# Kernel tuning notes

Measured on AMD Instinct MI355X. Metric: run time of the kernel, lower is better.

Reference implementation:

```python
import jax, jax.numpy as jnp
import numpy as np

N_HEAD = 16
HEAD_DIM = 64


def _shift(BD):
    # BD: [b, n, L, 2L] -> [b, n, L, L] (Transformer-XL left-shift trick)
    b, n, L, _ = BD.shape
    BD = jnp.pad(BD, ((0, 0), (0, 0), (0, 0), (0, 1)))          # [b,n,L,2L+1]
    BD = BD.reshape(b, n, 2 * L + 1, L)[:, :, :-1]              # [b,n,2L,L]
    BD = BD.reshape(b, n, L, 2 * L)[:, :, :, L:]                # [b,n,L,L]
    return BD


def _transpose_shift(E):
    # E: [b, n, L, 2L] -> [b, n, L, L]
    b, n, L, _ = E.shape
    E = jnp.pad(E, ((0, 0), (0, 0), (0, 0), (0, 1)))            # [b,n,L,2L+1]
    E = E.reshape(b, n, 2 * L + 1, L)                           # [b,n,2L+1,L]
    E = E[:, :, 1::2, :]                                        # rows 1,3,...,2L-1 -> [b,n,L,L]
    return E


def setup_inputs() -> dict:
    key = jax.random.key(0)
    ks = jax.random.split(key, 6)
    B, L, D = 4, 1024, 1024
    return {
        "x": jax.random.normal(ks[0], (B, L, D), jnp.float32),
        "pos_embed": jax.random.normal(ks[1], (2 * L, HEAD_DIM), jnp.float32),
        "W_qkv": jax.random.normal(ks[2], (D, 3 * D), jnp.float32) * (1.0 / np.sqrt(D)),
        "b_qkv": jax.random.normal(ks[3], (3 * D,), jnp.float32) * 0.01,
        "r_r_bias": jax.random.normal(ks[4], (N_HEAD, HEAD_DIM), jnp.float32) * 0.02,
        "r_w_bias": jax.random.normal(ks[5], (N_HEAD, HEAD_DIM), jnp.float32) * 0.02,
    }


def reference(x, pos_embed, W_qkv, b_qkv, r_r_bias, r_w_bias):
    b, L, d_model = x.shape
    scale = jnp.sqrt(jnp.asarray(HEAD_DIM, x.dtype))

    qkv = x @ W_qkv + b_qkv                                      # [b,L,3D]
    q, k, v = jnp.split(qkv, 3, axis=-1)

    def split_heads(t):  # [b,L,D] -> [b,n,L,hd]
        return t.reshape(b, L, N_HEAD, HEAD_DIM).transpose(0, 2, 1, 3)

    q, k, v = split_heads(q), split_heads(k), split_heads(v)

    rw_head_q = q + r_r_bias[None, :, None, :]
    AC = jnp.einsum('bnqd,bnkd->bnqk', rw_head_q, k)             # [b,n,L,L]
    D_ = jnp.einsum('nd,ld->nl', r_w_bias, pos_embed)[None, :, None, :]  # [1,n,1,2L]
    B_ = jnp.einsum('bnqd,ld->bnql', q, pos_embed)               # [b,n,L,2L]
    E_ = jnp.einsum('bnqd,ld->bnql', k, pos_embed)               # [b,n,L,2L]

    BDE = _shift(B_ + D_) + _transpose_shift(E_)
    attn = jax.nn.softmax((AC + BDE) / scale, axis=-1)

    out = jnp.einsum('bnqk,bnkd->bnqd', attn, v)                 # [b,n,L,hd]
    out = out.transpose(0, 2, 1, 3).reshape(b, L, d_model)       # merge heads
    return out
```

## Files before the change

kernel.cpp:

```cpp
#include <hip/hip_runtime.h>
#include <math.h>

typedef unsigned short u16;
typedef unsigned int u32;
typedef __attribute__((ext_vector_type(8))) short bf16x8;
typedef __attribute__((ext_vector_type(4))) float f32x4;

#define AS1 __attribute__((address_space(1)))
#define AS3 __attribute__((address_space(3)))

static __device__ __forceinline__ u16 f2b(float f) {
  u32 u = __float_as_uint(f);
  return (u16)((u + 0x7FFFu + ((u >> 16) & 1u)) >> 16);
}
static __device__ __forceinline__ u16 f2b_fast(float f) {
  return (u16)((__float_as_uint(f) + 0x8000u) >> 16);
}
static __device__ __forceinline__ float b2f(u16 b) {
  return __uint_as_float(((u32)b) << 16);
}

__global__ __launch_bounds__(256) void prep(
    const float* __restrict__ x, const float* __restrict__ W,
    const float* __restrict__ P,
    u16* __restrict__ xb, u16* __restrict__ Wt, u16* __restrict__ Pb)
{
  __shared__ u16 sT[64 * 68];
  const int bid = blockIdx.x, t = threadIdx.x;
  if (bid < 4096) {
    const size_t base = (size_t)bid * 1024 + t * 4;
    const float4 v = *(const float4*)(x + base);
    const u32 lo = (u32)f2b(v.x) | ((u32)f2b(v.y) << 16);
    const u32 hi = (u32)f2b(v.z) | ((u32)f2b(v.w) << 16);
    *(uint2*)(xb + base) = make_uint2(lo, hi);
  } else if (bid < 4224) {
    const size_t base = (size_t)(bid - 4096) * 1024 + t * 4;
    const float4 v = *(const float4*)(P + base);
    const u32 lo = (u32)f2b(v.x) | ((u32)f2b(v.y) << 16);
    const u32 hi = (u32)f2b(v.z) | ((u32)f2b(v.w) << 16);
    *(uint2*)(Pb + base) = make_uint2(lo, hi);
  } else if (bid < 4992) {
    const int tb = bid - 4224;
    const int tk = tb / 48, tn = tb % 48;
    const int k0 = tk * 64, n0 = tn * 64;
#pragma unroll
    for (int it = 0; it < 4; ++it) {
      const int c = it * 256 + t;
      const int r = c >> 4, c4 = (c & 15) << 2;
      const float4 v = *(const float4*)(W + (size_t)(k0 + r) * 3072 + n0 + c4);
      sT[(c4 + 0) * 68 + r] = f2b(v.x);
      sT[(c4 + 1) * 68 + r] = f2b(v.y);
      sT[(c4 + 2) * 68 + r] = f2b(v.z);
      sT[(c4 + 3) * 68 + r] = f2b(v.w);
    }
    __syncthreads();
#pragma unroll
    for (int it = 0; it < 4; ++it) {
      const int c = it * 256 + t;
      const int rr = c >> 4, k4 = (c & 15) << 2;
      const uint2 rv = *(const uint2*)(sT + rr * 68 + k4);
      *(uint2*)(Wt + (size_t)(n0 + rr) * 1024 + k0 + k4) = rv;
    }
  } else {
    if (t < 64) Pb[2048 * 64 + t] = f2b(P[2047 * 64 + t]);
  }
}

__global__ __launch_bounds__(256, 3) void qkv_gemm(
    const u16* __restrict__ xb, const u16* __restrict__ Wt,
    const float* __restrict__ bq,
    u16* __restrict__ Qh, u16* __restrict__ Kh, u16* __restrict__ Vt)
{
  __shared__ u16 smem[16384];
  u16* const sA = smem;
  u16* const sB = smem + 8192;
  u16* const T  = smem;
  u16* const Tv = smem;
  const int t = threadIdx.x;
  const int lane = t & 63, w = t >> 6;
  const int l = lane & 15, ql = lane >> 4;
  const int wm = w & 1, wn = w >> 1;
  const int vid = blockIdx.x;
  const int xcd = vid & 7, jj = vid >> 3;
  const int n0 = (xcd * 3 + (jj % 3)) * 128;
  const int m0 = (jj / 3) * 128;

  f32x4 acc[4][4];
#pragma unroll
  for (int i = 0; i < 4; ++i)
#pragma unroll
    for (int j = 0; j < 4; ++j) acc[i][j] = (f32x4){0.f, 0.f, 0.f, 0.f};

  for (int k0 = 0; k0 < 1024; k0 += 64) {
    __syncthreads();
#pragma unroll
    for (int j = 0; j < 4; ++j) {
      const int ii = w * 4 + j;
      const int m = ii * 8 + (lane >> 3);
      const int q8 = (lane & 7) ^ (m & 7);
      __builtin_amdgcn_global_load_lds(
          (const AS1 u32*)(xb + (size_t)(m0 + m) * 1024 + k0 + q8 * 8),
          (AS3 u32*)(sA + ii * 512), 16, 0, 0);
      __builtin_amdgcn_global_load_lds(
          (const AS1 u32*)(Wt + (size_t)(n0 + m) * 1024 + k0 + q8 * 8),
          (AS3 u32*)(sB + ii * 512), 16, 0, 0);
    }
    __syncthreads();
#pragma unroll
    for (int ks = 0; ks < 2; ++ks) {
      bf16x8 a[4], b[4];
#pragma unroll
      for (int mt = 0; mt < 4; ++mt) {
        const int m = wm * 64 + mt * 16 + l;
        a[mt] = *(const bf16x8*)(sA + m * 64 + (((ks * 4 + ql) ^ (m & 7)) * 8));
      }
#pragma unroll
      for (int nt = 0; nt < 4; ++nt) {
        const int nn = wn * 64 + nt * 16 + l;
        b[nt] = *(const bf16x8*)(sB + nn * 64 + (((ks * 4 + ql) ^ (nn & 7)) * 8));
      }
#pragma unroll
      for (int mt = 0; mt < 4; ++mt)
#pragma unroll
        for (int nt = 0; nt < 4; ++nt)
          acc[mt][nt] = __builtin_amdgcn_mfma_f32_16x16x32_bf16(
              a[mt], b[nt], acc[mt][nt], 0, 0, 0);
    }
  }

  const int which = n0 >> 10;
  const int qbase = m0 & 1023;
  const int bb = m0 >> 10;
  const int h0 = (n0 & 1023) >> 6;
#pragma unroll
  for (int pass = 0; pass < 2; ++pass) {
    __syncthreads();
    if (which < 2) {
      if (wm == pass) {
#pragma unroll
        for (int nt = 0; nt < 4; ++nt) {
          const int col = wn * 64 + nt * 16 + l;
          const float bias = bq[n0 + col];
#pragma unroll
          for (int mt = 0; mt < 4; ++mt)
#pragma unroll
            for (int rg = 0; rg < 4; ++rg)
              T[(mt * 16 + ql * 4 + rg) * 136 + col] = f2b(acc[mt][nt][rg] + bias);
        }
      }
      __syncthreads();
      u16* const dst = which ? Kh : Qh;
#pragma unroll
      for (int h = 0; h < 2; ++h) {
        const size_t bnoff = ((size_t)(bb * 16 + h0 + h)) << 16;
#pragma unroll
        for (int it = 0; it < 2; ++it) {
          const int c = it * 256 + t;
          const int r = c >> 3, d8 = (c & 7) * 8;
          const uint4 v = *(const uint4*)(T + r * 136 + h * 64 + d8);
          *(uint4*)(dst + bnoff + ((size_t)(qbase + pass * 64 + r) << 6) + d8) = v;
        }
      }
    } else {
      if (wm == pass) {
#pragma unroll
        for (int nt = 0; nt < 4; ++nt) {
          const int col = wn * 64 + nt * 16 + l;
          const float bias = bq[n0 + col];
#pragma unroll
          for (int mt = 0; mt < 4; ++mt) {
            const u32 lo = (u32)f2b(acc[mt][nt][0] + bias) |
                           ((u32)f2b(acc[mt][nt][1] + bias) << 16);
            const u32 hi = (u32)f2b(acc[mt][nt][2] + bias) |
                           ((u32)f2b(acc[mt][nt][3] + bias) << 16);
            *(uint2*)(Tv + col * 72 + mt * 16 + ql * 4) = make_uint2(lo, hi);
          }
        }
      }
      __syncthreads();
#pragma unroll
      for (int h = 0; h < 2; ++h) {
        const size_t bnoff = ((size_t)(bb * 16 + h0 + h)) << 16;
#pragma unroll
        for (int it = 0; it < 2; ++it) {
          const int c = it * 256 + t;
          const int dr = c >> 3, q8 = (c & 7) * 8;
          const uint4 v = *(const uint4*)(Tv + (h * 64 + dr) * 72 + q8);
          *(uint4*)(Vt + bnoff + ((size_t)dr << 10) + qbase + pass * 64 + q8) = v;
        }
      }
    }
  }
}

__global__ __launch_bounds__(256, 2) void rel_attn(
    const u16* __restrict__ Qh, const u16* __restrict__ Kh,
    const u16* __restrict__ Vt, const u16* __restrict__ Pb,
    const float* __restrict__ rrb, const float* __restrict__ rwb,
    float* __restrict__ out)
{
  __shared__ u16 smem[36864];
  u16* const sK    = smem;
  u16* const sVT   = smem + 8192;
  u16* const sPr   = smem + 16384;
  u16* const sProb = smem + 32768;
  u16* const sU    = smem;
  u16* const sW    = smem + 16384;

  const int t = threadIdx.x;
  const int lane = t & 63, w = t >> 6;
  const int l = lane & 15, ql = lane >> 4;
  const int vid = blockIdx.x;
  const int qt = vid >> 6, bn = vid & 63;
  const int n = bn & 15, bb = bn >> 4;
  const size_t hoff = (size_t)bn << 16;
  const int q0 = qt << 7;
  const int bz = 6 - 2 * w;

#pragma unroll
  for (int it = 0; it < 4; ++it) {
    const int c = it * 256 + t;
    const int i = c >> 3, ch = c & 7;
    const int d8 = ch * 8;
    const uint4 qv = *(const uint4*)(Qh + hoff + ((size_t)(q0 + i) << 6) + d8);
    const uint4 kv = *(const uint4*)(Kh + hoff + ((size_t)(q0 + i) << 6) + d8);
    const u16* qp = (const u16*)&qv;
    const u16* kp = (const u16*)&kv;
    u16 uo[8], wo[8];
#pragma unroll
    for (int e = 0; e < 8; ++e) {
      const float rv = rrb[n * 64 + d8 + e];
      const float wv = rwb[n * 64 + d8 + e];
      const float qf = b2f(qp[e]), kf = b2f(kp[e]);
      uo[e] = f2b(qf + rv);
      wo[e] = f2b(qf + wv + kf);
    }
    const int pos = i * 64 + ((ch ^ (i & 7)) * 8);
    *(uint4*)(sU + pos) = *(const uint4*)uo;
    *(uint4*)(sW + pos) = *(const uint4*)wo;
  }
  __syncthreads();

  bf16x8 au[2][2], aw[2][2];
#pragma unroll
  for (int mt = 0; mt < 2; ++mt)
#pragma unroll
    for (int ks = 0; ks < 2; ++ks) {
      const int row = w * 32 + mt * 16 + l;
      const int off = row * 64 + (((ks * 4 + ql) ^ (row & 7)) * 8);
      au[mt][ks] = *(const bf16x8*)(sU + off);
      aw[mt][ks] = *(const bf16x8*)(sW + off);
    }
  __syncthreads();

  {
#pragma unroll
    for (int j = 0; j < 2; ++j) {
      const int ii = w * 2 + j;
      const int m = ii * 8 + (lane >> 3);
      const int q8 = (lane & 7) ^ (m & 7);
      __builtin_amdgcn_global_load_lds(
          (const AS1 u32*)(Kh + hoff + ((size_t)m << 6) + q8 * 8),
          (AS3 u32*)(sK + ii * 512), 16, 0, 0);
      __builtin_amdgcn_global_load_lds(
          (const AS1 u32*)(Vt + hoff + ((size_t)m << 10) + q8 * 8),
          (AS3 u32*)(sVT + ii * 512), 16, 0, 0);
    }
    const int lbase0 = 897 - q0;
    const int rb0 = (896 - q0) & 255;
#pragma unroll
    for (int j = 0; j < 6; ++j) {
      const int ii = w * 6 + j;
      const int m = ii * 8 + (lane >> 3);
      const int q8 = (lane & 7) ^ (m & 7);
      __builtin_amdgcn_global_load_lds(
          (const AS1 u32*)(Pb + ((size_t)(lbase0 + m) << 6) + q8 * 8),
          (AS3 u32*)(sPr + ((rb0 + ii * 8) & 255) * 64), 16, 0, 0);
    }
  }

  const f32x4 Z0 = (f32x4){0.f, 0.f, 0.f, 0.f};
  f32x4 o[2][4];
  float lrun[2][4];
#pragma unroll
  for (int mt = 0; mt < 2; ++mt)
#pragma unroll
    for (int ii = 0; ii < 4; ++ii) {
      o[mt][ii] = (f32x4){0.f, 0.f, 0.f, 0.f};
      lrun[mt][ii] = 0.f;
    }

  for (int k0 = 0; k0 < 1024; k0 += 64) {
    const int cb = (k0 >> 6) & 1;
    const int rb = (896 + k0 - q0) & 255;
    __syncthreads();

    if (k0 < 960) {
      const int kn = k0 + 64;
#pragma unroll
      for (int j = 0; j < 2; ++j) {
        const int ii = w * 2 + j;
        const int m = ii * 8 + (lane >> 3);
        const int q8 = (lane & 7) ^ (m & 7);
        __builtin_amdgcn_global_load_lds(
            (const AS1 u32*)(Kh + hoff + ((size_t)(kn + m) << 6) + q8 * 8),
            (AS3 u32*)(sK + (cb ^ 1) * 4096 + ii * 512), 16, 0, 0);
        __builtin_amdgcn_global_load_lds(
            (const AS1 u32*)(Vt + hoff + ((size_t)m << 10) + kn + q8 * 8),
            (AS3 u32*)(sVT + (cb ^ 1) * 4096 + ii * 512), 16, 0, 0);
        __builtin_amdgcn_global_load_lds(
            (const AS1 u32*)(Pb + ((size_t)(897 + kn + 128 - q0 + m) << 6) + q8 * 8),
            (AS3 u32*)(sPr + ((rb + 192 + ii * 8) & 255) * 64), 16, 0, 0);
      }
    }

    const u16* const cK = sK + cb * 4096;
    const u16* const cV = sVT + cb * 4096;

    f32x4 z1[2][4], z2[2][5];
    __builtin_amdgcn_s_setprio(1);
#pragma unroll
    for (int ks = 0; ks < 2; ++ks) {
#pragma unroll
      for (int nt = 0; nt < 4; ++nt) {
        const int row = nt * 16 + l;
        const bf16x8 bk =
            *(const bf16x8*)(cK + row * 64 + (((ks * 4 + ql) ^ (row & 7)) * 8));
#pragma unroll
        for (int mt = 0; mt < 2; ++mt)
          z1[mt][nt] = __builtin_amdgcn_mfma_f32_16x16x32_bf16(
              au[mt][ks], bk, ks ? z1[mt][nt] : Z0, 0, 0, 0);
      }
#pragma unroll
      for (int rt = 0; rt < 6; ++rt) {
        const int row = (bz + rt) * 16 + l;
        const bf16x8 bp = *(const bf16x8*)(
            sPr + ((rb + row) & 255) * 64 + (((ks * 4 + ql) ^ (row & 7)) * 8));
        if (rt >= 1)
          z2[0][rt - 1] = __builtin_amdgcn_mfma_f32_16x16x32_bf16(
              aw[0][ks], bp, ks ? z2[0][rt - 1] : Z0, 0, 0, 0);
        if (rt <= 4)
          z2[1][rt] = __builtin_amdgcn_mfma_f32_16x16x32_bf16(
              aw[1][ks], bp, ks ? z2[1][rt] : Z0, 0, 0, 0);
      }
    }
    __builtin_amdgcn_s_setprio(0);

    float p[2][4][4];
#pragma unroll
    for (int mt = 0; mt < 2; ++mt)
#pragma unroll
      for (int ii = 0; ii < 4; ++ii) {
        const int ci = 15 - ql * 4 - ii;
        const int src = (lane & 48) | ((l + ci) & 15);
        const bool wrap = l < ci;
#pragma unroll
        for (int jt = 0; jt < 4; ++jt) {
          const float val = wrap ? z2[mt][jt + 1][ii] : z2[mt][jt][ii];
          const float g = __shfl(val, src, 64);
          const float pv =
              __builtin_amdgcn_exp2f((z1[mt][jt][ii] + g) * 0.18033688011112042f);
          p[mt][ii][jt] = pv;
          lrun[mt][ii] += pv;
        }
      }

#pragma unroll
    for (int ks = 0; ks < 2; ++ks) {
#pragma unroll
      for (int mt = 0; mt < 2; ++mt)
#pragma unroll
        for (int ii = 0; ii < 4; ++ii) {
          const int r = w * 32 + mt * 16 + ql * 4 + ii;
          const int sw2 = (r & 3) ^ ((r >> 2) & 3);
#pragma unroll
          for (int jh = 0; jh < 2; ++jh) {
            const int ch = jh * 2 + (l >> 3);
            sProb[r * 32 + ((ch ^ sw2) * 8) + (l & 7)] =
                f2b_fast(p[mt][ii][ks * 2 + jh]);
          }
        }
      bf16x8 bv[4];
#pragma unroll
      for (int dt = 0; dt < 4; ++dt) {
        const int row = dt * 16 + l;
        bv[dt] =
            *(const bf16x8*)(cV + row * 64 + (((ks * 4 + ql) ^ (row & 7)) * 8));
      }
      __builtin_amdgcn_s_setprio(1);
#pragma unroll
      for (int mt = 0; mt < 2; ++mt) {
        const int ar = w * 32 + mt * 16 + l;
        const bf16x8 ap = *(const bf16x8*)(
            sProb + ar * 32 + ((ql ^ ((ar & 3) ^ ((ar >> 2) & 3))) * 8));
#pragma unroll
        for (int dt = 0; dt < 4; ++dt)
          o[mt][dt] = __builtin_amdgcn_mfma_f32_16x16x32_bf16(
              ap, bv[dt], o[mt][dt], 0, 0, 0);
      }
      __builtin_amdgcn_s_setprio(0);
    }
  }

#pragma unroll
  for (int mt = 0; mt < 2; ++mt)
#pragma unroll
    for (int ii = 0; ii < 4; ++ii) {
      float ls = lrun[mt][ii];
      ls += __shfl_xor(ls, 1);
      ls += __shfl_xor(ls, 2);
      ls += __shfl_xor(ls, 4);
      ls += __shfl_xor(ls, 8);
      const float inv = 1.f / ls;
      const int q = q0 + w * 32 + mt * 16 + ql * 4 + ii;
#pragma unroll
      for (int dt = 0; dt < 4; ++dt)
        out[((size_t)(bb * 1024 + q) << 10) + (n << 6) + dt * 16 + l] =
            o[mt][dt][ii] * inv;
    }
}

extern "C" void kernel_launch(void* const* d_in, const int* in_sizes, int n_in,
                              void* d_out, int out_size, void* d_ws, size_t ws_size,
                              hipStream_t stream) {
  const float* x  = (const float*)d_in[0];
  const float* P  = (const float*)d_in[1];
  const float* Wq = (const float*)d_in[2];
  const float* bq = (const float*)d_in[3];
  const float* rr = (const float*)d_in[4];
  const float* rw = (const float*)d_in[5];
  float* out = (float*)d_out;

  char* ws = (char*)d_ws;
  u16* xb = (u16*)(ws);
  u16* Wt = (u16*)(ws + 8388608);
  u16* Pb = (u16*)(ws + 14680064);
  u16* Qh = (u16*)(ws + 14946304);
  u16* Kh = (u16*)(ws + 23334912);
  u16* Vt = (u16*)(ws + 31723520);

  prep<<<4993, 256, 0, stream>>>(x, Wq, P, xb, Wt, Pb);
  qkv_gemm<<<768, 256, 0, stream>>>(xb, Wt, bq, Qh, Kh, Vt);
  rel_attn<<<512, 256, 0, stream>>>(Qh, Kh, Vt, Pb, rr, rw, out);
}
```

Measured before the change: 172.1 us.

## Software-pipeline score MFMAs one key tile ahead of softmax and PV

Restructures the attention loop so the QK and positional score MFMAs for the next 64-key tile are issued while the current tile's exp and PV work runs, interleaved per k-slice. K and positional tiles are now prefetched two iterations ahead, with a prologue that loads two K tiles and computes the first tile's scores. V stays one tile ahead. The aim is to hide MFMA and LDS latency behind the softmax VALU work, at the cost of more live registers and subtler buffer-reuse ordering.

```diff
diff --git a/kernel.cpp b/kernel.cpp
--- a/kernel.cpp
+++ b/kernel.cpp
@@ -255,22 +255,30 @@
 
   {
 #pragma unroll
+    for (int b = 0; b < 2; ++b)
+#pragma unroll
+      for (int j = 0; j < 2; ++j) {
+        const int ii = w * 2 + j;
+        const int m = ii * 8 + (lane >> 3);
+        const int q8 = (lane & 7) ^ (m & 7);
+        __builtin_amdgcn_global_load_lds(
+            (const AS1 u32*)(Kh + hoff + ((size_t)(b * 64 + m) << 6) + q8 * 8),
+            (AS3 u32*)(sK + b * 4096 + ii * 512), 16, 0, 0);
+      }
+#pragma unroll
     for (int j = 0; j < 2; ++j) {
       const int ii = w * 2 + j;
       const int m = ii * 8 + (lane >> 3);
       const int q8 = (lane & 7) ^ (m & 7);
       __builtin_amdgcn_global_load_lds(
-          (const AS1 u32*)(Kh + hoff + ((size_t)m << 6) + q8 * 8),
-          (AS3 u32*)(sK + ii * 512), 16, 0, 0);
-      __builtin_amdgcn_global_load_lds(
           (const AS1 u32*)(Vt + hoff + ((size_t)m << 10) + q8 * 8),
           (AS3 u32*)(sVT + ii * 512), 16, 0, 0);
     }
     const int lbase0 = 897 - q0;
     const int rb0 = (896 - q0) & 255;
 #pragma unroll
-    for (int j = 0; j < 6; ++j) {
-      const int ii = w * 6 + j;
+    for (int j = 0; j < 8; ++j) {
+      const int ii = w * 8 + j;
       const int m = ii * 8 + (lane >> 3);
       const int q8 = (lane & 7) ^ (m & 7);
       __builtin_amdgcn_global_load_lds(
@@ -278,8 +286,39 @@
           (AS3 u32*)(sPr + ((rb0 + ii * 8) & 255) * 64), 16, 0, 0);
     }
   }
+  __syncthreads();
 
   const f32x4 Z0 = (f32x4){0.f, 0.f, 0.f, 0.f};
+  f32x4 z1[2][4], z2[2][5];
+  auto zhalf = [&](int kk, int ks, bool first) {
+    const u16* const cK = sK + (kk & 1) * 4096;
+    const int rbk = (896 + (kk << 6) - q0) & 255;
+#pragma unroll
+    for (int nt = 0; nt < 4; ++nt) {
+      const int row = nt * 16 + l;
+      const bf16x8 bk =
+          *(const bf16x8*)(cK + row * 64 + (((ks * 4 + ql) ^ (row & 7)) * 8));
+#pragma unroll
+      for (int mt = 0; mt < 2; ++mt)
+        z1[mt][nt] = __builtin_amdgcn_mfma_f32_16x16x32_bf16(
+            au[mt][ks], bk, first ? Z0 : z1[mt][nt], 0, 0, 0);
+    }
+#pragma unroll
+    for (int rt = 0; rt < 6; ++rt) {
+      const int row = (bz + rt) * 16 + l;
+      const bf16x8 bp = *(const bf16x8*)(
+          sPr + ((rbk + row) & 255) * 64 + (((ks * 4 + ql) ^ (row & 7)) * 8));
+      if (rt >= 1)
+        z2[0][rt - 1] = __builtin_amdgcn_mfma_f32_16x16x32_bf16(
+            aw[0][ks], bp, first ? Z0 : z2[0][rt - 1], 0, 0, 0);
+      if (rt <= 4)
+        z2[1][rt] = __builtin_amdgcn_mfma_f32_16x16x32_bf16(
+            aw[1][ks], bp, first ? Z0 : z2[1][rt], 0, 0, 0);
+    }
+  };
+  zhalf(0, 0, true);
+  zhalf(0, 1, false);
+
   f32x4 o[2][4];
   float lrun[2][4];
 #pragma unroll
@@ -290,61 +329,36 @@
       lrun[mt][ii] = 0.f;
     }
 
-  for (int k0 = 0; k0 < 1024; k0 += 64) {
-    const int cb = (k0 >> 6) & 1;
-    const int rb = (896 + k0 - q0) & 255;
+  for (int k = 0; k < 16; ++k) {
+    const int k0 = k << 6;
     __syncthreads();
 
-    if (k0 < 960) {
-      const int kn = k0 + 64;
+    const int rbk = (896 + k0 - q0) & 255;
+    if (k <= 13) {
 #pragma unroll
       for (int j = 0; j < 2; ++j) {
         const int ii = w * 2 + j;
         const int m = ii * 8 + (lane >> 3);
         const int q8 = (lane & 7) ^ (m & 7);
         __builtin_amdgcn_global_load_lds(
-            (const AS1 u32*)(Kh + hoff + ((size_t)(kn + m) << 6) + q8 * 8),
-            (AS3 u32*)(sK + (cb ^ 1) * 4096 + ii * 512), 16, 0, 0);
+            (const AS1 u32*)(Kh + hoff + ((size_t)(k0 + 128 + m) << 6) + q8 * 8),
+            (AS3 u32*)(sK + (k & 1) * 4096 + ii * 512), 16, 0, 0);
         __builtin_amdgcn_global_load_lds(
-            (const AS1 u32*)(Vt + hoff + ((size_t)m << 10) + kn + q8 * 8),
-            (AS3 u32*)(sVT + (cb ^ 1) * 4096 + ii * 512), 16, 0, 0);
+            (const AS1 u32*)(Pb + ((size_t)(897 + k0 + 256 - q0 + m) << 6) + q8 * 8),
+            (AS3 u32*)(sPr + ((rbk + ii * 8) & 255) * 64), 16, 0, 0);
+      }
+    }
+    if (k <= 14) {
+#pragma unroll
+      for (int j = 0; j < 2; ++j) {
+        const int ii = w * 2 + j;
+        const int m = ii * 8 + (lane >> 3);
+        const int q8 = (lane & 7) ^ (m & 7);
         __builtin_amdgcn_global_load_lds(
-            (const AS1 u32*)(Pb + ((size_t)(897 + kn + 128 - q0 + m) << 6) + q8 * 8),
-            (AS3 u32*)(sPr + ((rb + 192 + ii * 8) & 255) * 64), 16, 0, 0);
-      }
-    }
-
-    const u16* const cK = sK + cb * 4096;
-    const u16* const cV = sVT + cb * 4096;
-
-    f32x4 z1[2][4], z2[2][5];
-    __builtin_amdgcn_s_setprio(1);
-#pragma unroll
-    for (int ks = 0; ks < 2; ++ks) {
-#pragma unroll
-      for (int nt = 0; nt < 4; ++nt) {
-        const int row = nt * 16 + l;
-        const bf16x8 bk =
-            *(const bf16x8*)(cK + row * 64 + (((ks * 4 + ql) ^ (row & 7)) * 8));
-#pragma unroll
-        for (int mt = 0; mt < 2; ++mt)
-          z1[mt][nt] = __builtin_amdgcn_mfma_f32_16x16x32_bf16(
-              au[mt][ks], bk, ks ? z1[mt][nt] : Z0, 0, 0, 0);
-      }
-#pragma unroll
-      for (int rt = 0; rt < 6; ++rt) {
-        const int row = (bz + rt) * 16 + l;
-        const bf16x8 bp = *(const bf16x8*)(
-            sPr + ((rb + row) & 255) * 64 + (((ks * 4 + ql) ^ (row & 7)) * 8));
-        if (rt >= 1)
-          z2[0][rt - 1] = __builtin_amdgcn_mfma_f32_16x16x32_bf16(
-              aw[0][ks], bp, ks ? z2[0][rt - 1] : Z0, 0, 0, 0);
-        if (rt <= 4)
-          z2[1][rt] = __builtin_amdgcn_mfma_f32_16x16x32_bf16(
-              aw[1][ks], bp, ks ? z2[1][rt] : Z0, 0, 0, 0);
-      }
-    }
-    __builtin_amdgcn_s_setprio(0);
+            (const AS1 u32*)(Vt + hoff + ((size_t)m << 10) + k0 + 64 + q8 * 8),
+            (AS3 u32*)(sVT + ((k + 1) & 1) * 4096 + ii * 512), 16, 0, 0);
+      }
+    }
 
     float p[2][4][4];
 #pragma unroll
@@ -365,6 +379,7 @@
         }
       }
 
+    const u16* const cV = sVT + (k & 1) * 4096;
 #pragma unroll
     for (int ks = 0; ks < 2; ++ks) {
 #pragma unroll
@@ -380,6 +395,11 @@
                 f2b_fast(p[mt][ii][ks * 2 + jh]);
           }
         }
+      if (k < 15) {
+        __builtin_amdgcn_s_setprio(1);
+        zhalf(k + 1, ks, ks == 0);
+        __builtin_amdgcn_s_setprio(0);
+      }
       bf16x8 bv[4];
 #pragma unroll
       for (int dt = 0; dt < 4; ++dt) {
```

Result: faster. 163.5 us (-5.0%).

## Split attention block across eight waves with sixteen query rows each

Applied to the files above, without the earlier changes.

The relative attention kernel now launches 512 threads (8 waves) per block instead of 256, and each wave handles 16 query rows instead of 32. The K/V/P tile loads are redistributed over the extra waves, and the per-wave positional band shrinks from 6 to 5 row tiles. The aim is more latency hiding and less register pressure per wave. The cost is that each wave reuses the loaded K, V and P fragments for half as many rows, so LDS reads and shuffles per MFMA go up.

```diff
diff --git a/kernel.cpp b/kernel.cpp
--- a/kernel.cpp
+++ b/kernel.cpp
@@ -193,7 +193,7 @@
   }
 }
 
-__global__ __launch_bounds__(256, 2) void rel_attn(
+__global__ __launch_bounds__(512, 4) void rel_attn(
     const u16* __restrict__ Qh, const u16* __restrict__ Kh,
     const u16* __restrict__ Vt, const u16* __restrict__ Pb,
     const float* __restrict__ rrb, const float* __restrict__ rwb,
@@ -215,11 +215,11 @@
   const int n = bn & 15, bb = bn >> 4;
   const size_t hoff = (size_t)bn << 16;
   const int q0 = qt << 7;
-  const int bz = 6 - 2 * w;
-
-#pragma unroll
-  for (int it = 0; it < 4; ++it) {
-    const int c = it * 256 + t;
+  const int bz = 7 - w;
+
+#pragma unroll
+  for (int it = 0; it < 2; ++it) {
+    const int c = it * 512 + t;
     const int i = c >> 3, ch = c & 7;
     const int d8 = ch * 8;
     const uint4 qv = *(const uint4*)(Qh + hoff + ((size_t)(q0 + i) << 6) + d8);
@@ -241,54 +241,46 @@
   }
   __syncthreads();
 
-  bf16x8 au[2][2], aw[2][2];
-#pragma unroll
-  for (int mt = 0; mt < 2; ++mt)
-#pragma unroll
-    for (int ks = 0; ks < 2; ++ks) {
-      const int row = w * 32 + mt * 16 + l;
-      const int off = row * 64 + (((ks * 4 + ql) ^ (row & 7)) * 8);
-      au[mt][ks] = *(const bf16x8*)(sU + off);
-      aw[mt][ks] = *(const bf16x8*)(sW + off);
-    }
+  bf16x8 au[2], aw[2];
+#pragma unroll
+  for (int ks = 0; ks < 2; ++ks) {
+    const int row = w * 16 + l;
+    const int off = row * 64 + (((ks * 4 + ql) ^ (row & 7)) * 8);
+    au[ks] = *(const bf16x8*)(sU + off);
+    aw[ks] = *(const bf16x8*)(sW + off);
+  }
   __syncthreads();
 
   {
-#pragma unroll
-    for (int j = 0; j < 2; ++j) {
-      const int ii = w * 2 + j;
-      const int m = ii * 8 + (lane >> 3);
-      const int q8 = (lane & 7) ^ (m & 7);
-      __builtin_amdgcn_global_load_lds(
-          (const AS1 u32*)(Kh + hoff + ((size_t)m << 6) + q8 * 8),
-          (AS3 u32*)(sK + ii * 512), 16, 0, 0);
-      __builtin_amdgcn_global_load_lds(
-          (const AS1 u32*)(Vt + hoff + ((size_t)m << 10) + q8 * 8),
-          (AS3 u32*)(sVT + ii * 512), 16, 0, 0);
-    }
+    const int m = w * 8 + (lane >> 3);
+    const int q8 = (lane & 7) ^ (m & 7);
+    __builtin_amdgcn_global_load_lds(
+        (const AS1 u32*)(Kh + hoff + ((size_t)m << 6) + q8 * 8),
+        (AS3 u32*)(sK + w * 512), 16, 0, 0);
+    __builtin_amdgcn_global_load_lds(
+        (const AS1 u32*)(Vt + hoff + ((size_t)m << 10) + q8 * 8),
+        (AS3 u32*)(sVT + w * 512), 16, 0, 0);
     const int lbase0 = 897 - q0;
     const int rb0 = (896 - q0) & 255;
 #pragma unroll
-    for (int j = 0; j < 6; ++j) {
-      const int ii = w * 6 + j;
-      const int m = ii * 8 + (lane >> 3);
-      const int q8 = (lane & 7) ^ (m & 7);
-      __builtin_amdgcn_global_load_lds(
-          (const AS1 u32*)(Pb + ((size_t)(lbase0 + m) << 6) + q8 * 8),
+    for (int j = 0; j < 3; ++j) {
+      const int ii = w * 3 + j;
+      const int mm = ii * 8 + (lane >> 3);
+      const int qq = (lane & 7) ^ (mm & 7);
+      __builtin_amdgcn_global_load_lds(
+          (const AS1 u32*)(Pb + ((size_t)(lbase0 + mm) << 6) + qq * 8),
           (AS3 u32*)(sPr + ((rb0 + ii * 8) & 255) * 64), 16, 0, 0);
     }
   }
 
   const f32x4 Z0 = (f32x4){0.f, 0.f, 0.f, 0.f};
-  f32x4 o[2][4];
-  float lrun[2][4];
-#pragma unroll
-  for (int mt = 0; mt < 2; ++mt)
-#pragma unroll
-    for (int ii = 0; ii < 4; ++ii) {
-      o[mt][ii] = (f32x4){0.f, 0.f, 0.f, 0.f};
-      lrun[mt][ii] = 0.f;
-    }
+  f32x4 o[4];
+  float lrun[4];
+#pragma unroll
+  for (int ii = 0; ii < 4; ++ii) {
+    o[ii] = (f32x4){0.f, 0.f, 0.f, 0.f};
+    lrun[ii] = 0.f;
+  }
 
   for (int k0 = 0; k0 < 1024; k0 += 64) {
     const int cb = (k0 >> 6) & 1;
@@ -297,27 +289,23 @@
 
     if (k0 < 960) {
       const int kn = k0 + 64;
-#pragma unroll
-      for (int j = 0; j < 2; ++j) {
-        const int ii = w * 2 + j;
-        const int m = ii * 8 + (lane >> 3);
-        const int q8 = (lane & 7) ^ (m & 7);
-        __builtin_amdgcn_global_load_lds(
-            (const AS1 u32*)(Kh + hoff + ((size_t)(kn + m) << 6) + q8 * 8),
-            (AS3 u32*)(sK + (cb ^ 1) * 4096 + ii * 512), 16, 0, 0);
-        __builtin_amdgcn_global_load_lds(
-            (const AS1 u32*)(Vt + hoff + ((size_t)m << 10) + kn + q8 * 8),
-            (AS3 u32*)(sVT + (cb ^ 1) * 4096 + ii * 512), 16, 0, 0);
-        __builtin_amdgcn_global_load_lds(
-            (const AS1 u32*)(Pb + ((size_t)(897 + kn + 128 - q0 + m) << 6) + q8 * 8),
-            (AS3 u32*)(sPr + ((rb + 192 + ii * 8) & 255) * 64), 16, 0, 0);
-      }
+      const int m = w * 8 + (lane >> 3);
+      const int q8 = (lane & 7) ^ (m & 7);
+      __builtin_amdgcn_global_load_lds(
+          (const AS1 u32*)(Kh + hoff + ((size_t)(kn + m) << 6) + q8 * 8),
+          (AS3 u32*)(sK + (cb ^ 1) * 4096 + w * 512), 16, 0, 0);
+      __builtin_amdgcn_global_load_lds(
+          (const AS1 u32*)(Vt + hoff + ((size_t)m << 10) + kn + q8 * 8),
+          (AS3 u32*)(sVT + (cb ^ 1) * 4096 + w * 512), 16, 0, 0);
+      __builtin_amdgcn_global_load_lds(
+          (const AS1 u32*)(Pb + ((size_t)(897 + kn + 128 - q0 + m) << 6) + q8 * 8),
+          (AS3 u32*)(sPr + ((rb + 192 + w * 8) & 255) * 64), 16, 0, 0);
     }
 
     const u16* const cK = sK + cb * 4096;
     const u16* const cV = sVT + cb * 4096;
 
-    f32x4 z1[2][4], z2[2][5];
+    f32x4 z1[4], z2[5];
     __builtin_amdgcn_s_setprio(1);
 #pragma unroll
     for (int ks = 0; ks < 2; ++ks) {
@@ -326,60 +314,50 @@
         const int row = nt * 16 + l;
         const bf16x8 bk =
             *(const bf16x8*)(cK + row * 64 + (((ks * 4 + ql) ^ (row & 7)) * 8));
-#pragma unroll
-        for (int mt = 0; mt < 2; ++mt)
-          z1[mt][nt] = __builtin_amdgcn_mfma_f32_16x16x32_bf16(
-              au[mt][ks], bk, ks ? z1[mt][nt] : Z0, 0, 0, 0);
-      }
-#pragma unroll
-      for (int rt = 0; rt < 6; ++rt) {
+        z1[nt] = __builtin_amdgcn_mfma_f32_16x16x32_bf16(
+            au[ks], bk, ks ? z1[nt] : Z0, 0, 0, 0);
+      }
+#pragma unroll
+      for (int rt = 0; rt < 5; ++rt) {
         const int row = (bz + rt) * 16 + l;
         const bf16x8 bp = *(const bf16x8*)(
             sPr + ((rb + row) & 255) * 64 + (((ks * 4 + ql) ^ (row & 7)) * 8));
-        if (rt >= 1)
-          z2[0][rt - 1] = __builtin_amdgcn_mfma_f32_16x16x32_bf16(
-              aw[0][ks], bp, ks ? z2[0][rt - 1] : Z0, 0, 0, 0);
-        if (rt <= 4)
-          z2[1][rt] = __builtin_amdgcn_mfma_f32_16x16x32_bf16(
-              aw[1][ks], bp, ks ? z2[1][rt] : Z0, 0, 0, 0);
+        z2[rt] = __builtin_amdgcn_mfma_f32_16x16x32_bf16(
+            aw[ks], bp, ks ? z2[rt] : Z0, 0, 0, 0);
       }
     }
     __builtin_amdgcn_s_setprio(0);
 
-    float p[2][4][4];
-#pragma unroll
-    for (int mt = 0; mt < 2; ++mt)
+    float p[4][4];
+#pragma unroll
+    for (int ii = 0; ii < 4; ++ii) {
+      const int ci = 15 - ql * 4 - ii;
+      const int src = (lane & 48) | ((l + ci) & 15);
+      const bool wrap = l < ci;
+#pragma unroll
+      for (int jt = 0; jt < 4; ++jt) {
+        const float val = wrap ? z2[jt + 1][ii] : z2[jt][ii];
+        const float g = __shfl(val, src, 64);
+        const float pv =
+            __builtin_amdgcn_exp2f((z1[jt][ii] + g) * 0.18033688011112042f);
+        p[ii][jt] = pv;
+        lrun[ii] += pv;
+      }
+    }
+
+#pragma unroll
+    for (int ks = 0; ks < 2; ++ks) {
 #pragma unroll
       for (int ii = 0; ii < 4; ++ii) {
-        const int ci = 15 - ql * 4 - ii;
-        const int src = (lane & 48) | ((l + ci) & 15);
-        const bool wrap = l < ci;
-#pragma unroll
-        for (int jt = 0; jt < 4; ++jt) {
-          const float val = wrap ? z2[mt][jt + 1][ii] : z2[mt][jt][ii];
-          const float g = __shfl(val, src, 64);
-          const float pv =
-              __builtin_amdgcn_exp2f((z1[mt][jt][ii] + g) * 0.18033688011112042f);
-          p[mt][ii][jt] = pv;
-          lrun[mt][ii] += pv;
+        const int r = w * 16 + ql * 4 + ii;
+        const int sw2 = (r & 3) ^ ((r >> 2) & 3);
+#pragma unroll
+        for (int jh = 0; jh < 2; ++jh) {
+          const int ch = jh * 2 + (l >> 3);
+          sProb[r * 32 + ((ch ^ sw2) * 8) + (l & 7)] =
+              f2b_fast(p[ii][ks * 2 + jh]);
         }
       }
-
-#pragma unroll
-    for (int ks = 0; ks < 2; ++ks) {
-#pragma unroll
-      for (int mt = 0; mt < 2; ++mt)
-#pragma unroll
-        for (int ii = 0; ii < 4; ++ii) {
-          const int r = w * 32 + mt * 16 + ql * 4 + ii;
-          const int sw2 = (r & 3) ^ ((r >> 2) & 3);
-#pragma unroll
-          for (int jh = 0; jh < 2; ++jh) {
-            const int ch = jh * 2 + (l >> 3);
-            sProb[r * 32 + ((ch ^ sw2) * 8) + (l & 7)] =
-                f2b_fast(p[mt][ii][ks * 2 + jh]);
-          }
-        }
       bf16x8 bv[4];
 #pragma unroll
       for (int dt = 0; dt < 4; ++dt) {
@@ -388,36 +366,33 @@
             *(const bf16x8*)(cV + row * 64 + (((ks * 4 + ql) ^ (row & 7)) * 8));
       }
       __builtin_amdgcn_s_setprio(1);
-#pragma unroll
-      for (int mt = 0; mt < 2; ++mt) {
-        const int ar = w * 32 + mt * 16 + l;
+      {
+        const int ar = w * 16 + l;
         const bf16x8 ap = *(const bf16x8*)(
             sProb + ar * 32 + ((ql ^ ((ar & 3) ^ ((ar >> 2) & 3))) * 8));
 #pragma unroll
         for (int dt = 0; dt < 4; ++dt)
-          o[mt][dt] = __builtin_amdgcn_mfma_f32_16x16x32_bf16(
-              ap, bv[dt], o[mt][dt], 0, 0, 0);
+          o[dt] = __builtin_amdgcn_mfma_f32_16x16x32_bf16(
+              ap, bv[dt], o[dt], 0, 0, 0);
       }
       __builtin_amdgcn_s_setprio(0);
     }
   }
 
 #pragma unroll
-  for (int mt = 0; mt < 2; ++mt)
-#pragma unroll
-    for (int ii = 0; ii < 4; ++ii) {
-      float ls = lrun[mt][ii];
-      ls += __shfl_xor(ls, 1);
-      ls += __shfl_xor(ls, 2);
-      ls += __shfl_xor(ls, 4);
-      ls += __shfl_xor(ls, 8);
-      const float inv = 1.f / ls;
-      const int q = q0 + w * 32 + mt * 16 + ql * 4 + ii;
-#pragma unroll
-      for (int dt = 0; dt < 4; ++dt)
-        out[((size_t)(bb * 1024 + q) << 10) + (n << 6) + dt * 16 + l] =
-            o[mt][dt][ii] * inv;
-    }
+  for (int ii = 0; ii < 4; ++ii) {
+    float ls = lrun[ii];
+    ls += __shfl_xor(ls, 1);
+    ls += __shfl_xor(ls, 2);
+    ls += __shfl_xor(ls, 4);
+    ls += __shfl_xor(ls, 8);
+    const float inv = 1.f / ls;
+    const int q = q0 + w * 16 + ql * 4 + ii;
+#pragma unroll
+    for (int dt = 0; dt < 4; ++dt)
+      out[((size_t)(bb * 1024 + q) << 10) + (n << 6) + dt * 16 + l] =
+          o[dt][ii] * inv;
+  }
 }
 
 extern "C" void kernel_launch(void* const* d_in, const int* in_sizes, int n_in,
@@ -441,5 +416,5 @@
 
   prep<<<4993, 256, 0, stream>>>(x, Wq, P, xb, Wt, Pb);
   qkv_gemm<<<768, 256, 0, stream>>>(xb, Wt, bq, Qh, Kh, Vt);
-  rel_attn<<<512, 256, 0, stream>>>(Qh, Kh, Vt, Pb, rr, rw, out);
-}
+  rel_attn<<<512, 512, 0, stream>>>(Qh, Kh, Vt, Pb, rr, rw, out);
+}
```

New measurement: 170.5 us. Within noise of the previous version (-1.0%).

## Split key tile across wave pairs in rel_attn with 512-thread blocks

Applied to the files above, without the earlier changes.

Doubles the rel_attn block to 8 waves. Each pair of waves shares the same 32 query rows and splits each 64-key tile into two 32-key halves, each with its own probability buffer. Partial outputs and row sums are combined through shared memory at the end. This aims to raise wave-level parallelism per block and cut per-wave registers and MFMA work, at the cost of an extra reduction step, more shared memory, and redundant A-fragment loads.

```diff
diff --git a/kernel.cpp b/kernel.cpp
--- a/kernel.cpp
+++ b/kernel.cpp
@@ -193,13 +193,13 @@
   }
 }
 
-__global__ __launch_bounds__(256, 2) void rel_attn(
+__global__ __launch_bounds__(512, 4) void rel_attn(
     const u16* __restrict__ Qh, const u16* __restrict__ Kh,
     const u16* __restrict__ Vt, const u16* __restrict__ Pb,
     const float* __restrict__ rrb, const float* __restrict__ rwb,
     float* __restrict__ out)
 {
-  __shared__ u16 smem[36864];
+  __shared__ u16 smem[40960];
   u16* const sK    = smem;
   u16* const sVT   = smem + 8192;
   u16* const sPr   = smem + 16384;
@@ -210,16 +210,18 @@
   const int t = threadIdx.x;
   const int lane = t & 63, w = t >> 6;
   const int l = lane & 15, ql = lane >> 4;
+  const int wq = w >> 1, pw = w & 1;
   const int vid = blockIdx.x;
   const int qt = vid >> 6, bn = vid & 63;
   const int n = bn & 15, bb = bn >> 4;
   const size_t hoff = (size_t)bn << 16;
   const int q0 = qt << 7;
-  const int bz = 6 - 2 * w;
-
-#pragma unroll
-  for (int it = 0; it < 4; ++it) {
-    const int c = it * 256 + t;
+  const int bz2 = 6 - 2 * wq + 2 * pw;
+  u16* const sPb = sProb + pw * 4096;
+
+#pragma unroll
+  for (int it = 0; it < 2; ++it) {
+    const int c = it * 512 + t;
     const int i = c >> 3, ch = c & 7;
     const int d8 = ch * 8;
     const uint4 qv = *(const uint4*)(Qh + hoff + ((size_t)(q0 + i) << 6) + d8);
@@ -246,7 +248,7 @@
   for (int mt = 0; mt < 2; ++mt)
 #pragma unroll
     for (int ks = 0; ks < 2; ++ks) {
-      const int row = w * 32 + mt * 16 + l;
+      const int row = wq * 32 + mt * 16 + l;
       const int off = row * 64 + (((ks * 4 + ql) ^ (row & 7)) * 8);
       au[mt][ks] = *(const bf16x8*)(sU + off);
       aw[mt][ks] = *(const bf16x8*)(sW + off);
@@ -254,27 +256,23 @@
   __syncthreads();
 
   {
-#pragma unroll
-    for (int j = 0; j < 2; ++j) {
-      const int ii = w * 2 + j;
-      const int m = ii * 8 + (lane >> 3);
-      const int q8 = (lane & 7) ^ (m & 7);
-      __builtin_amdgcn_global_load_lds(
-          (const AS1 u32*)(Kh + hoff + ((size_t)m << 6) + q8 * 8),
-          (AS3 u32*)(sK + ii * 512), 16, 0, 0);
-      __builtin_amdgcn_global_load_lds(
-          (const AS1 u32*)(Vt + hoff + ((size_t)m << 10) + q8 * 8),
-          (AS3 u32*)(sVT + ii * 512), 16, 0, 0);
-    }
+    const int m = w * 8 + (lane >> 3);
+    const int q8 = (lane & 7) ^ (m & 7);
+    __builtin_amdgcn_global_load_lds(
+        (const AS1 u32*)(Kh + hoff + ((size_t)m << 6) + q8 * 8),
+        (AS3 u32*)(sK + w * 512), 16, 0, 0);
+    __builtin_amdgcn_global_load_lds(
+        (const AS1 u32*)(Vt + hoff + ((size_t)m << 10) + q8 * 8),
+        (AS3 u32*)(sVT + w * 512), 16, 0, 0);
     const int lbase0 = 897 - q0;
     const int rb0 = (896 - q0) & 255;
 #pragma unroll
-    for (int j = 0; j < 6; ++j) {
-      const int ii = w * 6 + j;
-      const int m = ii * 8 + (lane >> 3);
-      const int q8 = (lane & 7) ^ (m & 7);
-      __builtin_amdgcn_global_load_lds(
-          (const AS1 u32*)(Pb + ((size_t)(lbase0 + m) << 6) + q8 * 8),
+    for (int j = 0; j < 3; ++j) {
+      const int ii = w * 3 + j;
+      const int mm = ii * 8 + (lane >> 3);
+      const int qq = (lane & 7) ^ (mm & 7);
+      __builtin_amdgcn_global_load_lds(
+          (const AS1 u32*)(Pb + ((size_t)(lbase0 + mm) << 6) + qq * 8),
           (AS3 u32*)(sPr + ((rb0 + ii * 8) & 255) * 64), 16, 0, 0);
     }
   }
@@ -297,111 +295,103 @@
 
     if (k0 < 960) {
       const int kn = k0 + 64;
-#pragma unroll
-      for (int j = 0; j < 2; ++j) {
-        const int ii = w * 2 + j;
-        const int m = ii * 8 + (lane >> 3);
-        const int q8 = (lane & 7) ^ (m & 7);
-        __builtin_amdgcn_global_load_lds(
-            (const AS1 u32*)(Kh + hoff + ((size_t)(kn + m) << 6) + q8 * 8),
-            (AS3 u32*)(sK + (cb ^ 1) * 4096 + ii * 512), 16, 0, 0);
-        __builtin_amdgcn_global_load_lds(
-            (const AS1 u32*)(Vt + hoff + ((size_t)m << 10) + kn + q8 * 8),
-            (AS3 u32*)(sVT + (cb ^ 1) * 4096 + ii * 512), 16, 0, 0);
-        __builtin_amdgcn_global_load_lds(
-            (const AS1 u32*)(Pb + ((size_t)(897 + kn + 128 - q0 + m) << 6) + q8 * 8),
-            (AS3 u32*)(sPr + ((rb + 192 + ii * 8) & 255) * 64), 16, 0, 0);
-      }
+      const int m = w * 8 + (lane >> 3);
+      const int q8 = (lane & 7) ^ (m & 7);
+      __builtin_amdgcn_global_load_lds(
+          (const AS1 u32*)(Kh + hoff + ((size_t)(kn + m) << 6) + q8 * 8),
+          (AS3 u32*)(sK + (cb ^ 1) * 4096 + w * 512), 16, 0, 0);
+      __builtin_amdgcn_global_load_lds(
+          (const AS1 u32*)(Vt + hoff + ((size_t)m << 10) + kn + q8 * 8),
+          (AS3 u32*)(sVT + (cb ^ 1) * 4096 + w * 512), 16, 0, 0);
+      __builtin_amdgcn_global_load_lds(
+          (const AS1 u32*)(Pb + ((size_t)(897 + kn + 128 - q0 + m) << 6) + q8 * 8),
+          (AS3 u32*)(sPr + ((rb + 192 + w * 8) & 255) * 64), 16, 0, 0);
     }
 
     const u16* const cK = sK + cb * 4096;
     const u16* const cV = sVT + cb * 4096;
 
-    f32x4 z1[2][4], z2[2][5];
+    f32x4 z1[2][2], z2[2][3];
     __builtin_amdgcn_s_setprio(1);
 #pragma unroll
     for (int ks = 0; ks < 2; ++ks) {
 #pragma unroll
-      for (int nt = 0; nt < 4; ++nt) {
-        const int row = nt * 16 + l;
+      for (int jl = 0; jl < 2; ++jl) {
+        const int row = (2 * pw + jl) * 16 + l;
         const bf16x8 bk =
             *(const bf16x8*)(cK + row * 64 + (((ks * 4 + ql) ^ (row & 7)) * 8));
 #pragma unroll
         for (int mt = 0; mt < 2; ++mt)
-          z1[mt][nt] = __builtin_amdgcn_mfma_f32_16x16x32_bf16(
-              au[mt][ks], bk, ks ? z1[mt][nt] : Z0, 0, 0, 0);
-      }
-#pragma unroll
-      for (int rt = 0; rt < 6; ++rt) {
-        const int row = (bz + rt) * 16 + l;
+          z1[mt][jl] = __builtin_amdgcn_mfma_f32_16x16x32_bf16(
+              au[mt][ks], bk, ks ? z1[mt][jl] : Z0, 0, 0, 0);
+      }
+#pragma unroll
+      for (int v = 0; v < 4; ++v) {
+        const int row = (bz2 + v) * 16 + l;
         const bf16x8 bp = *(const bf16x8*)(
             sPr + ((rb + row) & 255) * 64 + (((ks * 4 + ql) ^ (row & 7)) * 8));
-        if (rt >= 1)
-          z2[0][rt - 1] = __builtin_amdgcn_mfma_f32_16x16x32_bf16(
-              aw[0][ks], bp, ks ? z2[0][rt - 1] : Z0, 0, 0, 0);
-        if (rt <= 4)
-          z2[1][rt] = __builtin_amdgcn_mfma_f32_16x16x32_bf16(
-              aw[1][ks], bp, ks ? z2[1][rt] : Z0, 0, 0, 0);
+        if (v >= 1)
+          z2[0][v - 1] = __builtin_amdgcn_mfma_f32_16x16x32_bf16(
+              aw[0][ks], bp, ks ? z2[0][v - 1] : Z0, 0, 0, 0);
+        if (v <= 2)
+          z2[1][v] = __builtin_amdgcn_mfma_f32_16x16x32_bf16(
+              aw[1][ks], bp, ks ? z2[1][v] : Z0, 0, 0, 0);
       }
     }
     __builtin_amdgcn_s_setprio(0);
 
-    float p[2][4][4];
-#pragma unroll
-    for (int mt = 0; mt < 2; ++mt)
+#pragma unroll
+    for (int mt = 0; mt < 2; ++mt) {
+      float p[4][2];
 #pragma unroll
       for (int ii = 0; ii < 4; ++ii) {
         const int ci = 15 - ql * 4 - ii;
         const int src = (lane & 48) | ((l + ci) & 15);
         const bool wrap = l < ci;
 #pragma unroll
-        for (int jt = 0; jt < 4; ++jt) {
-          const float val = wrap ? z2[mt][jt + 1][ii] : z2[mt][jt][ii];
+        for (int jl = 0; jl < 2; ++jl) {
+          const float val = wrap ? z2[mt][jl + 1][ii] : z2[mt][jl][ii];
           const float g = __shfl(val, src, 64);
           const float pv =
-              __builtin_amdgcn_exp2f((z1[mt][jt][ii] + g) * 0.18033688011112042f);
-          p[mt][ii][jt] = pv;
+              __builtin_amdgcn_exp2f((z1[mt][jl][ii] + g) * 0.18033688011112042f);
+          p[ii][jl] = pv;
           lrun[mt][ii] += pv;
         }
       }
-
-#pragma unroll
-    for (int ks = 0; ks < 2; ++ks) {
-#pragma unroll
-      for (int mt = 0; mt < 2; ++mt)
-#pragma unroll
-        for (int ii = 0; ii < 4; ++ii) {
-          const int r = w * 32 + mt * 16 + ql * 4 + ii;
-          const int sw2 = (r & 3) ^ ((r >> 2) & 3);
-#pragma unroll
-          for (int jh = 0; jh < 2; ++jh) {
-            const int ch = jh * 2 + (l >> 3);
-            sProb[r * 32 + ((ch ^ sw2) * 8) + (l & 7)] =
-                f2b_fast(p[mt][ii][ks * 2 + jh]);
-          }
-        }
-      bf16x8 bv[4];
-#pragma unroll
-      for (int dt = 0; dt < 4; ++dt) {
-        const int row = dt * 16 + l;
-        bv[dt] =
-            *(const bf16x8*)(cV + row * 64 + (((ks * 4 + ql) ^ (row & 7)) * 8));
-      }
-      __builtin_amdgcn_s_setprio(1);
-#pragma unroll
-      for (int mt = 0; mt < 2; ++mt) {
-        const int ar = w * 32 + mt * 16 + l;
-        const bf16x8 ap = *(const bf16x8*)(
-            sProb + ar * 32 + ((ql ^ ((ar & 3) ^ ((ar >> 2) & 3))) * 8));
-#pragma unroll
-        for (int dt = 0; dt < 4; ++dt)
-          o[mt][dt] = __builtin_amdgcn_mfma_f32_16x16x32_bf16(
-              ap, bv[dt], o[mt][dt], 0, 0, 0);
-      }
-      __builtin_amdgcn_s_setprio(0);
-    }
-  }
-
+#pragma unroll
+      for (int ii = 0; ii < 4; ++ii) {
+        const int r = wq * 32 + mt * 16 + ql * 4 + ii;
+        const int sw2 = (r & 3) ^ ((r >> 2) & 3);
+#pragma unroll
+        for (int jl = 0; jl < 2; ++jl) {
+          const int ch = jl * 2 + (l >> 3);
+          sPb[r * 32 + ((ch ^ sw2) * 8) + (l & 7)] = f2b_fast(p[ii][jl]);
+        }
+      }
+    }
+
+    bf16x8 bv[4];
+#pragma unroll
+    for (int dt = 0; dt < 4; ++dt) {
+      const int row = dt * 16 + l;
+      bv[dt] =
+          *(const bf16x8*)(cV + row * 64 + (((pw * 4 + ql) ^ (row & 7)) * 8));
+    }
+    __builtin_amdgcn_s_setprio(1);
+#pragma unroll
+    for (int mt = 0; mt < 2; ++mt) {
+      const int ar = wq * 32 + mt * 16 + l;
+      const bf16x8 ap = *(const bf16x8*)(
+          sPb + ar * 32 + ((ql ^ ((ar & 3) ^ ((ar >> 2) & 3))) * 8));
+#pragma unroll
+      for (int dt = 0; dt < 4; ++dt)
+        o[mt][dt] = __builtin_amdgcn_mfma_f32_16x16x32_bf16(
+            ap, bv[dt], o[mt][dt], 0, 0, 0);
+    }
+    __builtin_amdgcn_s_setprio(0);
+  }
+
+  float lsum[2][4];
 #pragma unroll
   for (int mt = 0; mt < 2; ++mt)
 #pragma unroll
@@ -411,13 +401,45 @@
       ls += __shfl_xor(ls, 2);
       ls += __shfl_xor(ls, 4);
       ls += __shfl_xor(ls, 8);
-      const float inv = 1.f / ls;
-      const int q = q0 + w * 32 + mt * 16 + ql * 4 + ii;
+      lsum[mt][ii] = ls;
+    }
+  __syncthreads();
+  float* const fb = (float*)smem;
+  float* const fl = fb + 8192;
+  if (pw == 1) {
+#pragma unroll
+    for (int mt = 0; mt < 2; ++mt)
 #pragma unroll
       for (int dt = 0; dt < 4; ++dt)
-        out[((size_t)(bb * 1024 + q) << 10) + (n << 6) + dt * 16 + l] =
-            o[mt][dt][ii] * inv;
-    }
+#pragma unroll
+        for (int ii = 0; ii < 4; ++ii)
+          fb[wq * 2048 + (mt * 16 + ql * 4 + ii) * 64 + dt * 16 + l] =
+              o[mt][dt][ii];
+    if (l == 0)
+#pragma unroll
+      for (int mt = 0; mt < 2; ++mt)
+#pragma unroll
+        for (int ii = 0; ii < 4; ++ii)
+          fl[wq * 32 + mt * 16 + ql * 4 + ii] = lsum[mt][ii];
+  }
+  __syncthreads();
+  if (pw == 0) {
+#pragma unroll
+    for (int mt = 0; mt < 2; ++mt)
+#pragma unroll
+      for (int ii = 0; ii < 4; ++ii) {
+        const int r32 = mt * 16 + ql * 4 + ii;
+        const float inv = 1.f / (lsum[mt][ii] + fl[wq * 32 + r32]);
+        const int q = q0 + wq * 32 + r32;
+#pragma unroll
+        for (int dt = 0; dt < 4; ++dt) {
+          const float val =
+              o[mt][dt][ii] + fb[wq * 2048 + r32 * 64 + dt * 16 + l];
+          out[((size_t)(bb * 1024 + q) << 10) + (n << 6) + dt * 16 + l] =
+              val * inv;
+        }
+      }
+  }
 }
 
 extern "C" void kernel_launch(void* const* d_in, const int* in_sizes, int n_in,
@@ -441,5 +463,5 @@
 
   prep<<<4993, 256, 0, stream>>>(x, Wq, P, xb, Wt, Pb);
   qkv_gemm<<<768, 256, 0, stream>>>(xb, Wt, bq, Qh, Kh, Vt);
-  rel_attn<<<512, 256, 0, stream>>>(Qh, Kh, Vt, Pb, rr, rw, out);
-}
+  rel_attn<<<512, 512, 0, stream>>>(Qh, Kh, Vt, Pb, rr, rw, out);
+}
```

Result: slower. 229.9 us (+33.6%).
